# Kernel tuning notes

Hardware: AMD Instinct MI355X
Metric: run time of the kernel (lower is better)

Reference implementation:

```python
import jax, jax.numpy as jnp
import numpy as np

IN_F = 512
OUT_F = 256
ALPHA = 0.2  # LeakyReLU negative slope
NEG_INF = -9e15


def setup_inputs() -> dict:
    key = jax.random.key(0)
    k1, k2, k3, k4 = jax.random.split(key, 4)
    N = 8192
    inp = jax.random.normal(k1, (N, IN_F), dtype=jnp.float32)
    adj = jax.random.randint(k2, (N, N), 0, 2, dtype=jnp.int32)
    # xavier_normal with gain=1.414
    std_W = 1.414 * np.sqrt(2.0 / (IN_F + OUT_F))
    W = jax.random.normal(k3, (IN_F, OUT_F), dtype=jnp.float32) * std_W
    std_a = 1.414 * np.sqrt(2.0 / (2 * OUT_F + 1))
    a = jax.random.normal(k4, (2 * OUT_F, 1), dtype=jnp.float32) * std_a
    return {"input": inp, "adj": adj, "W": W, "a": a}


def reference(input, adj, W, a):
    h = input @ W                              # [N, F]
    attn_self = h @ a[:OUT_F]                  # [N, 1]
    attn_neigh = h @ a[OUT_F:]                 # [N, 1]
    dense = attn_self + attn_neigh.T           # [N, N] broadcast add
    dense = jnp.where(dense >= 0, dense, ALPHA * dense)  # leaky relu
    scores = jnp.where(adj > 0, dense, NEG_INF)
    attention = jax.nn.softmax(scores, axis=1)  # dropout p=0.0 -> identity
    h_prime = attention @ h                     # [N, F]
    return jax.nn.elu(h_prime)                  # concat=True branch
```

## Files before the change

### kernel.cpp

```cpp
#include <hip/hip_runtime.h>
#include <hip/hip_bf16.h>
#include <math.h>

#define DEVI static __device__ __forceinline__

using f32x4  = __attribute__((ext_vector_type(4))) float;
using f32x16 = __attribute__((ext_vector_type(16))) float;
using s16x8  = __attribute__((ext_vector_type(8))) short;
using bf16x8 = __attribute__((ext_vector_type(8))) __bf16;
using i32x4  = __attribute__((ext_vector_type(4))) int;
using u32x2  = __attribute__((ext_vector_type(2))) unsigned int;
using u32x4  = __attribute__((ext_vector_type(4))) unsigned int;

constexpr int N   = 8192;
constexpr int KIN = 512;
constexpr int F   = 256;

DEVI unsigned f2bf(float f) {
  unsigned u = __builtin_bit_cast(unsigned, f);
  return ((u + 0x7FFFu + ((u >> 16) & 1u)) >> 16) & 0xFFFFu;
}

DEVI float bfLO(unsigned u) { return __builtin_bit_cast(float, (u & 0xFFFFu) << 16); }
DEVI float bfHI(unsigned u) { return __builtin_bit_cast(float, u & 0xFFFF0000u); }

DEVI unsigned cvtpk(float lo, float hi) {
  unsigned r;
  asm("v_cvt_pk_bf16_f32 %0, %1, %2" : "=v"(r) : "v"(lo), "v"(hi));
  return r;
}

DEVI f32x16 mfma32(s16x8 a, s16x8 b, f32x16 c) {
  return __builtin_amdgcn_mfma_f32_32x32x16_bf16(
      __builtin_bit_cast(bf16x8, a), __builtin_bit_cast(bf16x8, b), c, 0, 0, 0);
}

DEVI void gload16(const void* g, void* lds_uniform) {
  __builtin_amdgcn_global_load_lds(
      (const __attribute__((address_space(1))) unsigned*)g,
      (__attribute__((address_space(3))) unsigned*)lds_uniform, 16, 0, 0);
}

__global__ __launch_bounds__(256) void k_prep_w(const float* __restrict__ W,
                                                unsigned short* __restrict__ Wt) {
  int t = blockIdx.x * 256 + threadIdx.x;
  int c = t >> 6, k0 = (t & 63) * 8;
  s16x8 o;
#pragma unroll
  for (int i = 0; i < 8; ++i) o[i] = (short)f2bf(W[(size_t)(k0 + i) * F + c]);
  *(s16x8*)(Wt + (size_t)c * KIN + k0) = o;
}

__global__ __launch_bounds__(512) void k_gemm1(const float* __restrict__ input,
                                               const unsigned short* __restrict__ Wt,
                                               const float* __restrict__ a_vec,
                                               unsigned short* __restrict__ Hj,
                                               float* __restrict__ E, float* __restrict__ E5,
                                               unsigned* __restrict__ FG) {
  __shared__ __align__(16) char lds[8192 + 32768 + 2048];
  char* ldsA = lds;
  char* ldsW = lds + 8192;
  float* red = (float*)(lds + 8192 + 32768);
  int tid = threadIdx.x, w = tid >> 6, l = tid & 63;
  int r0 = blockIdx.x * 32;
  f32x16 acc;
#pragma unroll
  for (int i = 0; i < 16; ++i) acc[i] = 0.f;

  int lrow8 = l >> 3;
  int koffB = ((l & 7) ^ lrow8) * 8;
  int ra = l & 31, kb = (l >> 5) * 8;
  int colw = w * 32 + ra;

  const int arow = tid >> 4, ac16 = tid & 15;
  const int aoff = (ac16 * 4) ^ ((arow & 7) << 2);
  const float* aR = input + (size_t)(r0 + arow) * KIN + aoff;

  for (int it = 0; it < 8; ++it) {
    int k0 = it * 64;
    __syncthreads();
    gload16(aR + k0, ldsA + w * 1024);
#pragma unroll
    for (int qi = 0; qi < 4; ++qi) {
      int q = 4 * w + qi;
      int c = 8 * q + lrow8;
      gload16(Wt + (size_t)c * KIN + k0 + koffB, ldsW + q * 1024);
    }
    __syncthreads();
    s16x8 av[4], bv[4];
#pragma unroll
    for (int kf = 0; kf < 4; ++kf) {
      int e4 = (kf * 16 + kb) * 4;
      f32x4 a0 = *(const f32x4*)(ldsA + ra * 256 + (e4 ^ ((ra & 7) << 4)));
      f32x4 a1 = *(const f32x4*)(ldsA + ra * 256 + ((e4 + 16) ^ ((ra & 7) << 4)));
      u32x4 ap;
      ap[0] = cvtpk(a0[0], a0[1]); ap[1] = cvtpk(a0[2], a0[3]);
      ap[2] = cvtpk(a1[0], a1[1]); ap[3] = cvtpk(a1[2], a1[3]);
      av[kf] = __builtin_bit_cast(s16x8, ap);
      int kk2 = (kf * 16 + kb) * 2;
      bv[kf] = *(const s16x8*)(ldsW + colw * 128 + (kk2 ^ ((colw & 7) << 4)));
    }
#pragma unroll
    for (int kf = 0; kf < 4; ++kf) acc = mfma32(av[kf], bv[kf], acc);
  }

  float a1v = a_vec[colw], a2v = a_vec[256 + colw];
  int rquad = (l >> 5) * 4;
#pragma unroll
  for (int g = 0; g < 4; ++g) {
    int jj = r0 + g * 8 + rquad;
    unsigned h0 = f2bf(acc[g * 4 + 0]), h1 = f2bf(acc[g * 4 + 1]);
    unsigned h2 = f2bf(acc[g * 4 + 2]), h3 = f2bf(acc[g * 4 + 3]);
    u32x2 pk;
    pk[0] = h0 | (h1 << 16);
    pk[1] = h2 | (h3 << 16);
    *(u32x2*)(Hj + ((size_t)(jj >> 4)) * 4096 + colw * 16 + (jj & 15)) = pk;
  }
#pragma unroll
  for (int g = 0; g < 16; ++g) {
    float vs = acc[g] * a1v;
    float vn = acc[g] * a2v;
#pragma unroll
    for (int m = 1; m <= 16; m <<= 1) {
      vs += __shfl_xor(vs, m, 64);
      vn += __shfl_xor(vn, m, 64);
    }
    if ((l & 31) == 0) {
      int row = (g & 3) + 8 * (g >> 2) + rquad;
      red[row * 8 + w] = vs;
      red[256 + row * 8 + w] = vn;
    }
  }
  __syncthreads();
  if (tid < 32) {
    float s = 0.f, n2 = 0.f;
#pragma unroll
    for (int i = 0; i < 8; ++i) { s += red[tid * 8 + i]; n2 += red[256 + tid * 8 + i]; }
    E[r0 + tid]  = expf(s);
    E5[r0 + tid] = expf(0.2f * s);
    FG[r0 + tid] = f2bf(expf(n2)) | (f2bf(expf(0.2f * n2)) << 16);
  }
}

__global__ __launch_bounds__(512, 4) void k_phase2(const int* __restrict__ adj,
                                                   const unsigned short* __restrict__ Hj,
                                                   const float* __restrict__ E,
                                                   const float* __restrict__ E5,
                                                   const unsigned* __restrict__ FG,
                                                   unsigned short* __restrict__ pacc,
                                                   float* __restrict__ ps) {
  __shared__ __align__(16) char ldsP[8192];

  const int tid = threadIdx.x, w = tid >> 6, l = tid & 63;
  const int rb = blockIdx.x >> 2, ks = blockIdx.x & 3;
  const int r0 = rb * 64;
  const int jb = ks * 2048;

  const int r = tid >> 3, jc8 = (tid & 7) * 8;
  const float Er = E[r0 + r], E5r = E5[r0 + r];
  float s_part = 0.f;
  const int*      __restrict__ adjR = adj + (size_t)(r0 + r) * N + jb + jc8;
  const unsigned* __restrict__ fgR  = FG + jb + jc8;
  const int pw_byte = r * 128 + ((jc8 * 2) ^ ((r & 7) << 4));

  const int rg = w & 1, cp = w >> 1;
  const int ra = rg * 32 + (l & 31);
  const int khb = (l >> 5) * 16;
  const int colb = cp * 64 + (l & 31);
  const int swzA = (ra & 7) << 4;
  const int kh8 = (l >> 5) * 8;
  const unsigned short* __restrict__ HjB =
      Hj + (size_t)(jb >> 4) * 4096 + colb * 16 + kh8;

  f32x16 acc0, acc1;
#pragma unroll
  for (int i = 0; i < 16; ++i) { acc0[i] = 0.f; acc1[i] = 0.f; }

  i32x4 ad0 = *(const i32x4*)(adjR);
  i32x4 ad1 = *(const i32x4*)(adjR + 4);
  u32x4 fc0 = *(const u32x4*)(fgR);
  u32x4 fc1 = *(const u32x4*)(fgR + 4);

  for (int it = 0; it < 32; ++it) {
    const int jn = ((it + 1) & 31) * 64;
    const unsigned short* hb = HjB + (size_t)it * 16384;

    s16x8 b00 = *(const s16x8*)(hb);
    s16x8 b01 = *(const s16x8*)(hb + 512);
    s16x8 b10 = *(const s16x8*)(hb + 4096);
    s16x8 b11 = *(const s16x8*)(hb + 4096 + 512);
    s16x8 b20 = *(const s16x8*)(hb + 8192);
    s16x8 b21 = *(const s16x8*)(hb + 8192 + 512);
    s16x8 b30 = *(const s16x8*)(hb + 12288);
    s16x8 b31 = *(const s16x8*)(hb + 12288 + 512);

    {
      float p0 = (ad0[0] != 0) ? fmaxf(Er * bfLO(fc0[0]), E5r * bfHI(fc0[0])) : 0.f;
      float p1 = (ad0[1] != 0) ? fmaxf(Er * bfLO(fc0[1]), E5r * bfHI(fc0[1])) : 0.f;
      float p2 = (ad0[2] != 0) ? fmaxf(Er * bfLO(fc0[2]), E5r * bfHI(fc0[2])) : 0.f;
      float p3 = (ad0[3] != 0) ? fmaxf(Er * bfLO(fc0[3]), E5r * bfHI(fc0[3])) : 0.f;
      float p4 = (ad1[0] != 0) ? fmaxf(Er * bfLO(fc1[0]), E5r * bfHI(fc1[0])) : 0.f;
      float p5 = (ad1[1] != 0) ? fmaxf(Er * bfLO(fc1[1]), E5r * bfHI(fc1[1])) : 0.f;
      float p6 = (ad1[2] != 0) ? fmaxf(Er * bfLO(fc1[2]), E5r * bfHI(fc1[2])) : 0.f;
      float p7 = (ad1[3] != 0) ? fmaxf(Er * bfLO(fc1[3]), E5r * bfHI(fc1[3])) : 0.f;
      s_part += ((p0 + p1) + (p2 + p3)) + ((p4 + p5) + (p6 + p7));
      u32x4 pk;
      pk[0] = cvtpk(p0, p1); pk[1] = cvtpk(p2, p3);
      pk[2] = cvtpk(p4, p5); pk[3] = cvtpk(p6, p7);
      *(u32x4*)(ldsP + pw_byte) = pk;
    }

    ad0 = *(const i32x4*)(adjR + jn);
    ad1 = *(const i32x4*)(adjR + jn + 4);
    fc0 = *(const u32x4*)(fgR + jn);
    fc1 = *(const u32x4*)(fgR + jn + 4);

    asm volatile("s_waitcnt lgkmcnt(0)" ::: "memory");
    __builtin_amdgcn_s_barrier();

    {
      s16x8 av0 = *(const s16x8*)(ldsP + ra * 128 + ((0 * 32 + khb) ^ swzA));
      s16x8 av1 = *(const s16x8*)(ldsP + ra * 128 + ((1 * 32 + khb) ^ swzA));
      s16x8 av2 = *(const s16x8*)(ldsP + ra * 128 + ((2 * 32 + khb) ^ swzA));
      s16x8 av3 = *(const s16x8*)(ldsP + ra * 128 + ((3 * 32 + khb) ^ swzA));
      __builtin_amdgcn_s_setprio(1);
      acc0 = mfma32(av0, b00, acc0);
      acc1 = mfma32(av0, b01, acc1);
      acc0 = mfma32(av1, b10, acc0);
      acc1 = mfma32(av1, b11, acc1);
      acc0 = mfma32(av2, b20, acc0);
      acc1 = mfma32(av2, b21, acc1);
      acc0 = mfma32(av3, b30, acc0);
      acc1 = mfma32(av3, b31, acc1);
      __builtin_amdgcn_s_setprio(0);
    }

    asm volatile("s_waitcnt lgkmcnt(0)" ::: "memory");
    __builtin_amdgcn_s_barrier();
  }

  float s = s_part;
#pragma unroll
  for (int m = 1; m <= 4; m <<= 1) s += __shfl_xor(s, m, 64);
  if ((tid & 7) == 0) ps[(size_t)ks * N + r0 + r] = s;

  unsigned short* po = pacc + (size_t)ks * N * F;
#pragma unroll
  for (int g = 0; g < 16; ++g) {
    int orow = rg * 32 + (g & 3) + 8 * (g >> 2) + 4 * (l >> 5);
    unsigned short* pr = po + (size_t)(r0 + orow) * F + colb;
    pr[0]  = (unsigned short)f2bf(acc0[g]);
    pr[32] = (unsigned short)f2bf(acc1[g]);
  }
}

__global__ __launch_bounds__(256) void k_combine(const unsigned short* __restrict__ pacc,
                                                 const float* __restrict__ ps,
                                                 float* __restrict__ out) {
  int t = blockIdx.x * 256 + threadIdx.x;
  size_t idx = (size_t)t * 4;
  int row = (int)(idx >> 8);
  f32x4 sum;
#pragma unroll
  for (int i = 0; i < 4; ++i) sum[i] = 0.f;
#pragma unroll
  for (int k = 0; k < 4; ++k) {
    u32x2 q = *(const u32x2*)(pacc + (size_t)k * N * F + idx);
    sum[0] += bfLO(q[0]); sum[1] += bfHI(q[0]);
    sum[2] += bfLO(q[1]); sum[3] += bfHI(q[1]);
  }
  float inv = 1.f / (ps[row] + ps[N + row] + ps[2 * N + row] + ps[3 * N + row]);
  f32x4 o;
#pragma unroll
  for (int i = 0; i < 4; ++i) {
    float v = sum[i] * inv;
    o[i] = v > 0.f ? v : expm1f(v);
  }
  *(f32x4*)(out + idx) = o;
}

extern "C" void kernel_launch(void* const* d_in, const int* in_sizes, int n_in,
                              void* d_out, int out_size, void* d_ws, size_t ws_size,
                              hipStream_t stream) {
  const float* input = (const float*)d_in[0];
  const int*   adj   = (const int*)d_in[1];
  const float* W     = (const float*)d_in[2];
  const float* a     = (const float*)d_in[3];
  float* out = (float*)d_out;
  char* ws = (char*)d_ws;

  unsigned short* pacc = (unsigned short*)(ws);
  unsigned short* Wt   = (unsigned short*)(ws + 8388608);
  unsigned short* Hj   = (unsigned short*)(ws + 16777216);
  float*    E  = (float*)(ws + 20971520);
  float*    E5 = (float*)(ws + 21004288);
  unsigned* FG = (unsigned*)(ws + 21037056);
  float*    ps = (float*)(ws + 21069824);

  hipLaunchKernelGGL(k_prep_w, dim3(64),   dim3(256), 0, stream, W, Wt);
  hipLaunchKernelGGL(k_gemm1,  dim3(256),  dim3(512), 0, stream, input, Wt, a, Hj, E, E5, FG);
  hipLaunchKernelGGL(k_phase2, dim3(512),  dim3(512), 0, stream, adj, Hj, E, E5, FG, pacc, ps);
  hipLaunchKernelGGL(k_combine,dim3(2048), dim3(256), 0, stream, pacc, ps, out);
}
```

Before: 113.1 us.

## Double the K-step per iteration and stage B-fragment loads across MFMA groups

The phase-2 loop now handles 128 neighbor columns per iteration instead of 64. This halves the iteration count and the number of barrier pairs, and doubles the LDS P tile with a wider swizzle. The H fragment global loads are split into staged groups placed between MFMA batches, so fewer B registers are live at once and load latency overlaps compute. The cost is more adj/FG registers per thread and twice the LDS per block, which could reduce occupancy at 4 blocks per CU.

```diff
diff --git a/kernel.cpp b/kernel.cpp
--- a/kernel.cpp
+++ b/kernel.cpp
@@ -149,25 +149,27 @@
                                                    const unsigned* __restrict__ FG,
                                                    unsigned short* __restrict__ pacc,
                                                    float* __restrict__ ps) {
-  __shared__ __align__(16) char ldsP[8192];
+  __shared__ __align__(16) char ldsP[16384];
 
   const int tid = threadIdx.x, w = tid >> 6, l = tid & 63;
   const int rb = blockIdx.x >> 2, ks = blockIdx.x & 3;
   const int r0 = rb * 64;
   const int jb = ks * 2048;
 
-  const int r = tid >> 3, jc8 = (tid & 7) * 8;
+  const int r = tid >> 3, jc16 = (tid & 7) * 16;
   const float Er = E[r0 + r], E5r = E5[r0 + r];
   float s_part = 0.f;
-  const int*      __restrict__ adjR = adj + (size_t)(r0 + r) * N + jb + jc8;
-  const unsigned* __restrict__ fgR  = FG + jb + jc8;
-  const int pw_byte = r * 128 + ((jc8 * 2) ^ ((r & 7) << 4));
+  const int*      __restrict__ adjR = adj + (size_t)(r0 + r) * N + jb + jc16;
+  const unsigned* __restrict__ fgR  = FG + jb + jc16;
+  const int pswz = (r & 15) << 4;
+  const int pw0 = r * 256 + ((jc16 * 2) ^ pswz);
+  const int pw1 = r * 256 + ((jc16 * 2 + 16) ^ pswz);
 
   const int rg = w & 1, cp = w >> 1;
   const int ra = rg * 32 + (l & 31);
   const int khb = (l >> 5) * 16;
   const int colb = cp * 64 + (l & 31);
-  const int swzA = (ra & 7) << 4;
+  const int swzA = (ra & 15) << 4;
   const int kh8 = (l >> 5) * 8;
   const unsigned short* __restrict__ HjB =
       Hj + (size_t)(jb >> 4) * 4096 + colb * 16 + kh8;
@@ -178,60 +180,110 @@
 
   i32x4 ad0 = *(const i32x4*)(adjR);
   i32x4 ad1 = *(const i32x4*)(adjR + 4);
+  i32x4 ad2 = *(const i32x4*)(adjR + 8);
+  i32x4 ad3 = *(const i32x4*)(adjR + 12);
   u32x4 fc0 = *(const u32x4*)(fgR);
   u32x4 fc1 = *(const u32x4*)(fgR + 4);
-
-  for (int it = 0; it < 32; ++it) {
-    const int jn = ((it + 1) & 31) * 64;
-    const unsigned short* hb = HjB + (size_t)it * 16384;
+  u32x4 fc2 = *(const u32x4*)(fgR + 8);
+  u32x4 fc3 = *(const u32x4*)(fgR + 12);
+
+  for (int it = 0; it < 16; ++it) {
+    const int jn = ((it + 1) & 15) * 128;
+    const unsigned short* hb = HjB + (size_t)it * 32768;
 
     s16x8 b00 = *(const s16x8*)(hb);
     s16x8 b01 = *(const s16x8*)(hb + 512);
     s16x8 b10 = *(const s16x8*)(hb + 4096);
     s16x8 b11 = *(const s16x8*)(hb + 4096 + 512);
-    s16x8 b20 = *(const s16x8*)(hb + 8192);
-    s16x8 b21 = *(const s16x8*)(hb + 8192 + 512);
-    s16x8 b30 = *(const s16x8*)(hb + 12288);
-    s16x8 b31 = *(const s16x8*)(hb + 12288 + 512);
 
     {
-      float p0 = (ad0[0] != 0) ? fmaxf(Er * bfLO(fc0[0]), E5r * bfHI(fc0[0])) : 0.f;
-      float p1 = (ad0[1] != 0) ? fmaxf(Er * bfLO(fc0[1]), E5r * bfHI(fc0[1])) : 0.f;
-      float p2 = (ad0[2] != 0) ? fmaxf(Er * bfLO(fc0[2]), E5r * bfHI(fc0[2])) : 0.f;
-      float p3 = (ad0[3] != 0) ? fmaxf(Er * bfLO(fc0[3]), E5r * bfHI(fc0[3])) : 0.f;
-      float p4 = (ad1[0] != 0) ? fmaxf(Er * bfLO(fc1[0]), E5r * bfHI(fc1[0])) : 0.f;
-      float p5 = (ad1[1] != 0) ? fmaxf(Er * bfLO(fc1[1]), E5r * bfHI(fc1[1])) : 0.f;
-      float p6 = (ad1[2] != 0) ? fmaxf(Er * bfLO(fc1[2]), E5r * bfHI(fc1[2])) : 0.f;
-      float p7 = (ad1[3] != 0) ? fmaxf(Er * bfLO(fc1[3]), E5r * bfHI(fc1[3])) : 0.f;
+      float p0, p1, p2, p3, p4, p5, p6, p7;
+      u32x4 pka, pkb;
+      p0 = (ad0[0] != 0) ? fmaxf(Er * bfLO(fc0[0]), E5r * bfHI(fc0[0])) : 0.f;
+      p1 = (ad0[1] != 0) ? fmaxf(Er * bfLO(fc0[1]), E5r * bfHI(fc0[1])) : 0.f;
+      p2 = (ad0[2] != 0) ? fmaxf(Er * bfLO(fc0[2]), E5r * bfHI(fc0[2])) : 0.f;
+      p3 = (ad0[3] != 0) ? fmaxf(Er * bfLO(fc0[3]), E5r * bfHI(fc0[3])) : 0.f;
+      p4 = (ad1[0] != 0) ? fmaxf(Er * bfLO(fc1[0]), E5r * bfHI(fc1[0])) : 0.f;
+      p5 = (ad1[1] != 0) ? fmaxf(Er * bfLO(fc1[1]), E5r * bfHI(fc1[1])) : 0.f;
+      p6 = (ad1[2] != 0) ? fmaxf(Er * bfLO(fc1[2]), E5r * bfHI(fc1[2])) : 0.f;
+      p7 = (ad1[3] != 0) ? fmaxf(Er * bfLO(fc1[3]), E5r * bfHI(fc1[3])) : 0.f;
       s_part += ((p0 + p1) + (p2 + p3)) + ((p4 + p5) + (p6 + p7));
-      u32x4 pk;
-      pk[0] = cvtpk(p0, p1); pk[1] = cvtpk(p2, p3);
-      pk[2] = cvtpk(p4, p5); pk[3] = cvtpk(p6, p7);
-      *(u32x4*)(ldsP + pw_byte) = pk;
+      pka[0] = cvtpk(p0, p1); pka[1] = cvtpk(p2, p3);
+      pka[2] = cvtpk(p4, p5); pka[3] = cvtpk(p6, p7);
+      p0 = (ad2[0] != 0) ? fmaxf(Er * bfLO(fc2[0]), E5r * bfHI(fc2[0])) : 0.f;
+      p1 = (ad2[1] != 0) ? fmaxf(Er * bfLO(fc2[1]), E5r * bfHI(fc2[1])) : 0.f;
+      p2 = (ad2[2] != 0) ? fmaxf(Er * bfLO(fc2[2]), E5r * bfHI(fc2[2])) : 0.f;
+      p3 = (ad2[3] != 0) ? fmaxf(Er * bfLO(fc2[3]), E5r * bfHI(fc2[3])) : 0.f;
+      p4 = (ad3[0] != 0) ? fmaxf(Er * bfLO(fc3[0]), E5r * bfHI(fc3[0])) : 0.f;
+      p5 = (ad3[1] != 0) ? fmaxf(Er * bfLO(fc3[1]), E5r * bfHI(fc3[1])) : 0.f;
+      p6 = (ad3[2] != 0) ? fmaxf(Er * bfLO(fc3[2]), E5r * bfHI(fc3[2])) : 0.f;
+      p7 = (ad3[3] != 0) ? fmaxf(Er * bfLO(fc3[3]), E5r * bfHI(fc3[3])) : 0.f;
+      s_part += ((p0 + p1) + (p2 + p3)) + ((p4 + p5) + (p6 + p7));
+      pkb[0] = cvtpk(p0, p1); pkb[1] = cvtpk(p2, p3);
+      pkb[2] = cvtpk(p4, p5); pkb[3] = cvtpk(p6, p7);
+      *(u32x4*)(ldsP + pw0) = pka;
+      *(u32x4*)(ldsP + pw1) = pkb;
     }
 
     ad0 = *(const i32x4*)(adjR + jn);
     ad1 = *(const i32x4*)(adjR + jn + 4);
+    ad2 = *(const i32x4*)(adjR + jn + 8);
+    ad3 = *(const i32x4*)(adjR + jn + 12);
     fc0 = *(const u32x4*)(fgR + jn);
     fc1 = *(const u32x4*)(fgR + jn + 4);
+    fc2 = *(const u32x4*)(fgR + jn + 8);
+    fc3 = *(const u32x4*)(fgR + jn + 12);
 
     asm volatile("s_waitcnt lgkmcnt(0)" ::: "memory");
     __builtin_amdgcn_s_barrier();
 
     {
-      s16x8 av0 = *(const s16x8*)(ldsP + ra * 128 + ((0 * 32 + khb) ^ swzA));
-      s16x8 av1 = *(const s16x8*)(ldsP + ra * 128 + ((1 * 32 + khb) ^ swzA));
-      s16x8 av2 = *(const s16x8*)(ldsP + ra * 128 + ((2 * 32 + khb) ^ swzA));
-      s16x8 av3 = *(const s16x8*)(ldsP + ra * 128 + ((3 * 32 + khb) ^ swzA));
+      s16x8 b20 = *(const s16x8*)(hb + 8192);
+      s16x8 b21 = *(const s16x8*)(hb + 8192 + 512);
+      s16x8 b30 = *(const s16x8*)(hb + 12288);
+      s16x8 b31 = *(const s16x8*)(hb + 12288 + 512);
+      s16x8 a0 = *(const s16x8*)(ldsP + ra * 256 + ((0 * 32 + khb) ^ swzA));
+      s16x8 a1 = *(const s16x8*)(ldsP + ra * 256 + ((1 * 32 + khb) ^ swzA));
       __builtin_amdgcn_s_setprio(1);
-      acc0 = mfma32(av0, b00, acc0);
-      acc1 = mfma32(av0, b01, acc1);
-      acc0 = mfma32(av1, b10, acc0);
-      acc1 = mfma32(av1, b11, acc1);
-      acc0 = mfma32(av2, b20, acc0);
-      acc1 = mfma32(av2, b21, acc1);
-      acc0 = mfma32(av3, b30, acc0);
-      acc1 = mfma32(av3, b31, acc1);
+      acc0 = mfma32(a0, b00, acc0);
+      acc1 = mfma32(a0, b01, acc1);
+      acc0 = mfma32(a1, b10, acc0);
+      acc1 = mfma32(a1, b11, acc1);
+      __builtin_amdgcn_s_setprio(0);
+
+      s16x8 b40 = *(const s16x8*)(hb + 16384);
+      s16x8 b41 = *(const s16x8*)(hb + 16384 + 512);
+      s16x8 b50 = *(const s16x8*)(hb + 20480);
+      s16x8 b51 = *(const s16x8*)(hb + 20480 + 512);
+      s16x8 a2 = *(const s16x8*)(ldsP + ra * 256 + ((2 * 32 + khb) ^ swzA));
+      s16x8 a3 = *(const s16x8*)(ldsP + ra * 256 + ((3 * 32 + khb) ^ swzA));
+      __builtin_amdgcn_s_setprio(1);
+      acc0 = mfma32(a2, b20, acc0);
+      acc1 = mfma32(a2, b21, acc1);
+      acc0 = mfma32(a3, b30, acc0);
+      acc1 = mfma32(a3, b31, acc1);
+      __builtin_amdgcn_s_setprio(0);
+
+      s16x8 b60 = *(const s16x8*)(hb + 24576);
+      s16x8 b61 = *(const s16x8*)(hb + 24576 + 512);
+      s16x8 b70 = *(const s16x8*)(hb + 28672);
+      s16x8 b71 = *(const s16x8*)(hb + 28672 + 512);
+      s16x8 a4 = *(const s16x8*)(ldsP + ra * 256 + ((4 * 32 + khb) ^ swzA));
+      s16x8 a5 = *(const s16x8*)(ldsP + ra * 256 + ((5 * 32 + khb) ^ swzA));
+      __builtin_amdgcn_s_setprio(1);
+      acc0 = mfma32(a4, b40, acc0);
+      acc1 = mfma32(a4, b41, acc1);
+      acc0 = mfma32(a5, b50, acc0);
+      acc1 = mfma32(a5, b51, acc1);
+      __builtin_amdgcn_s_setprio(0);
+
+      s16x8 a6 = *(const s16x8*)(ldsP + ra * 256 + ((6 * 32 + khb) ^ swzA));
+      s16x8 a7 = *(const s16x8*)(ldsP + ra * 256 + ((7 * 32 + khb) ^ swzA));
+      __builtin_amdgcn_s_setprio(1);
+      acc0 = mfma32(a6, b60, acc0);
+      acc1 = mfma32(a6, b61, acc1);
+      acc0 = mfma32(a7, b70, acc0);
+      acc1 = mfma32(a7, b71, acc1);
       __builtin_amdgcn_s_setprio(0);
     }
 
```

After: 116.7 us. +3.2%, slower.
